# Kernel tuning notes

Hardware: AMD Instinct MI355X
Metric: run time of the kernel (lower is better)

## Reference

```python
import jax, jax.numpy as jnp
import numpy as np

LN_EPS = 1e-5  # torch LayerNorm default
K_NN = 5       # top-5 nearest patterns (simple-surprise path)


def setup_inputs() -> dict:
    key = jax.random.key(0)
    ks = jax.random.split(key, 5)
    B, S, D, M = 8, 8192, 256, 50
    return {
        "hidden_states": jax.random.normal(ks[0], (B, S, D), dtype=jnp.float32),
        "memory": jax.random.normal(ks[1], (M, D), dtype=jnp.float32),
        "W1": jax.random.normal(ks[2], (D, 2 * D), dtype=jnp.float32) * (1.0 / np.sqrt(D)),
        "b1": jnp.zeros((2 * D,), dtype=jnp.float32),
        "W2": jax.random.normal(ks[3], (2 * D, D), dtype=jnp.float32) * (1.0 / np.sqrt(2 * D)),
        "b2": jnp.zeros((D,), dtype=jnp.float32),
        "ln_gamma": jnp.ones((D,), dtype=jnp.float32),
        "ln_beta": jnp.zeros((D,), dtype=jnp.float32),
    }


def reference(hidden_states, memory, W1, b1, W2, b2, ln_gamma, ln_beta):
    # Feature extractor: Linear -> ReLU -> (Dropout, eval=identity) -> Linear -> LayerNorm
    h = jax.nn.relu(jnp.einsum("bsd,de->bse", hidden_states, W1) + b1)
    f = jnp.einsum("bse,ed->bsd", h, W2) + b2
    mu = jnp.mean(f, axis=-1, keepdims=True)
    var = jnp.var(f, axis=-1, keepdims=True)
    feats = (f - mu) * jax.lax.rsqrt(var + LN_EPS) * ln_gamma + ln_beta  # [B,S,D]

    # Simple-surprise path, vectorized over all (b, s) tokens:
    # L2 distance of each token feature to every memory pattern.
    f_sq = jnp.sum(feats * feats, axis=-1)      # [B,S]
    m_sq = jnp.sum(memory * memory, axis=-1)    # [M]
    dots = jnp.einsum("bsd,md->bsm", feats, memory)  # [B,S,M]
    d2 = jnp.maximum(f_sq[..., None] + m_sq - 2.0 * dots, 0.0)
    dists = jnp.sqrt(d2)                        # [B,S,M]

    # k smallest distances -> mean -> sigmoid(avg - 1)
    neg_knn, _ = jax.lax.top_k(-dists, K_NN)    # [B,S,K]
    avg_dist = -jnp.mean(neg_knn, axis=-1)      # [B,S]
    surprise_scores = jax.nn.sigmoid(avg_dist - 1.0)
    return surprise_scores
```

## Files before the change

kernel.cpp:

```cpp
#include <hip/hip_runtime.h>
#include <math.h>

typedef __attribute__((ext_vector_type(8))) short bf16x8;
typedef __attribute__((ext_vector_type(4))) float f32x4;

static __device__ __forceinline__ unsigned short f2b(float x) {
  unsigned int u = __float_as_uint(x);
  u += 0x7FFFu + ((u >> 16) & 1u);
  return (unsigned short)(u >> 16);
}

__global__ void prep_weights(const float* __restrict__ W1,
                             const float* __restrict__ W2,
                             const float* __restrict__ mem,
                             unsigned short* __restrict__ W1T,
                             unsigned short* __restrict__ W2T,
                             unsigned short* __restrict__ memB,
                             float* __restrict__ msq) {
  int i = blockIdx.x * 256 + threadIdx.x;
  if (i < 131072) {
    int k = i >> 9, n = i & 511;
    W1T[n * 256 + k] = f2b(W1[i]);
  } else if (i < 262144) {
    int j = i - 131072;
    int k = j >> 8, n = j & 255;
    W2T[n * 512 + k] = f2b(W2[j]);
  } else if (i < 278528) {
    int j = i - 262144;
    int r = j >> 8;
    memB[j] = (r < 50) ? f2b(mem[j]) : (unsigned short)0;
  } else {
    int t = threadIdx.x;
    int r = t >> 2, c0 = (t & 3) * 64;
    float s = 0.f;
    if (r < 50) {
      for (int c = 0; c < 64; ++c) {
        float v = mem[r * 256 + c0 + c];
        s += v * v;
      }
    }
    s += __shfl_xor(s, 1, 64);
    s += __shfl_xor(s, 2, 64);
    if ((t & 3) == 0) msq[r] = (r < 50) ? s : 1e30f;
  }
}

#define XP 264
#define HP 136
#define DPitch 53

__global__ __launch_bounds__(256, 3) void fused_main(
    const float* __restrict__ X, const float* __restrict__ b1v,
    const float* __restrict__ b2v, const float* __restrict__ gammav,
    const float* __restrict__ betav, const unsigned short* __restrict__ W1T,
    const unsigned short* __restrict__ W2T,
    const unsigned short* __restrict__ memB, const float* __restrict__ msq,
    float* __restrict__ out) {
  __shared__ __align__(16) char smem[51200];
  unsigned short* Xs = (unsigned short*)smem;
  unsigned short* Hs = (unsigned short*)(smem + 33792);
  float* distS = (float*)(smem + 33792);
  float* red = (float*)(smem + 47360);
  float* psum   = red;
  float* psumsq = red + 256;
  float* fsqp   = red + 512;
  float* muS    = red + 768;
  float* rstdS  = red + 832;
  float* fsqS   = red + 896;

  const int tid = threadIdx.x;
  const int wid = tid >> 6;
  const int lane = tid & 63;
  const int l16 = lane & 15;
  const int quad = lane >> 4;

  const float4* X4 = (const float4*)(X + (size_t)blockIdx.x * 64 * 256);
#pragma unroll
  for (int j = 0; j < 16; ++j) {
    int idx = j * 256 + tid;
    float4 v = X4[idx];
    int row = idx >> 6, c4 = (idx & 63) << 2;
    unsigned int p0 = f2b(v.x) | ((unsigned int)f2b(v.y) << 16);
    unsigned int p1 = f2b(v.z) | ((unsigned int)f2b(v.w) << 16);
    *(uint2*)(&Xs[row * XP + c4]) = make_uint2(p0, p1);
  }

  f32x4 acc2[4][4];
#pragma unroll
  for (int mt = 0; mt < 4; ++mt) {
    const float4 bb = *(const float4*)(&b2v[wid * 64 + mt * 16 + quad * 4]);
#pragma unroll
    for (int nt = 0; nt < 4; ++nt) {
      acc2[mt][nt][0] = bb.x; acc2[mt][nt][1] = bb.y;
      acc2[mt][nt][2] = bb.z; acc2[mt][nt][3] = bb.w;
    }
  }

  __syncthreads();

  for (int cc = 0; cc < 4; ++cc) {
    int hbase = cc * 128 + wid * 32;
    f32x4 acc1[2][4];
#pragma unroll
    for (int mt = 0; mt < 2; ++mt) {
      const float4 bb = *(const float4*)(&b1v[hbase + mt * 16 + quad * 4]);
#pragma unroll
      for (int nt = 0; nt < 4; ++nt) {
        acc1[mt][nt][0] = bb.x; acc1[mt][nt][1] = bb.y;
        acc1[mt][nt][2] = bb.z; acc1[mt][nt][3] = bb.w;
      }
    }
    bf16x8 a2p[2][4];
#pragma unroll
    for (int k2 = 0; k2 < 2; ++k2)
#pragma unroll
      for (int mt = 0; mt < 4; ++mt)
        a2p[k2][mt] = *(const bf16x8*)(W2T + (wid * 64 + mt * 16 + l16) * 512 +
                                       cc * 128 + k2 * 32 + quad * 8);
#pragma unroll
    for (int kk = 0; kk < 8; ++kk) {
      int k0 = kk * 32 + quad * 8;
      bf16x8 a[2], b[4];
#pragma unroll
      for (int mt = 0; mt < 2; ++mt)
        a[mt] = *(const bf16x8*)(W1T + (hbase + mt * 16 + l16) * 256 + k0);
#pragma unroll
      for (int nt = 0; nt < 4; ++nt)
        b[nt] = *(const bf16x8*)(Xs + (nt * 16 + l16) * XP + k0);
#pragma unroll
      for (int mt = 0; mt < 2; ++mt)
#pragma unroll
        for (int nt = 0; nt < 4; ++nt)
          acc1[mt][nt] = __builtin_amdgcn_mfma_f32_16x16x32_bf16(
              a[mt], b[nt], acc1[mt][nt], 0, 0, 0);
    }
    __syncthreads();
#pragma unroll
    for (int mt = 0; mt < 2; ++mt) {
#pragma unroll
      for (int nt = 0; nt < 4; ++nt) {
        int token = nt * 16 + l16;
        int hloc = wid * 32 + mt * 16 + quad * 4;
        f32x4 v = acc1[mt][nt];
        unsigned int p0 = f2b(fmaxf(v[0], 0.f)) | ((unsigned int)f2b(fmaxf(v[1], 0.f)) << 16);
        unsigned int p1 = f2b(fmaxf(v[2], 0.f)) | ((unsigned int)f2b(fmaxf(v[3], 0.f)) << 16);
        *(uint2*)(&Hs[token * HP + hloc]) = make_uint2(p0, p1);
      }
    }
    __syncthreads();
#pragma unroll
    for (int k2 = 0; k2 < 4; ++k2) {
      int k0 = k2 * 32 + quad * 8;
      bf16x8 a[4], b[4];
#pragma unroll
      for (int mt = 0; mt < 4; ++mt) {
        if (k2 < 2)
          a[mt] = a2p[k2][mt];
        else
          a[mt] = *(const bf16x8*)(W2T + (wid * 64 + mt * 16 + l16) * 512 +
                                   cc * 128 + k0 - quad * 8 + quad * 8);
      }
#pragma unroll
      for (int nt = 0; nt < 4; ++nt)
        b[nt] = *(const bf16x8*)(Hs + (nt * 16 + l16) * HP + k0);
#pragma unroll
      for (int mt = 0; mt < 4; ++mt)
#pragma unroll
        for (int nt = 0; nt < 4; ++nt)
          acc2[mt][nt] = __builtin_amdgcn_mfma_f32_16x16x32_bf16(
              a[mt], b[nt], acc2[mt][nt], 0, 0, 0);
    }
  }

  __syncthreads();

#pragma unroll
  for (int nt = 0; nt < 4; ++nt) {
    float s = 0.f, sq = 0.f;
#pragma unroll
    for (int mt = 0; mt < 4; ++mt)
#pragma unroll
      for (int r = 0; r < 4; ++r) {
        float v = acc2[mt][nt][r];
        s += v; sq += v * v;
      }
    s += __shfl_xor(s, 16, 64); sq += __shfl_xor(sq, 16, 64);
    s += __shfl_xor(s, 32, 64); sq += __shfl_xor(sq, 32, 64);
    if (quad == 0) {
      psum[wid * 64 + nt * 16 + l16] = s;
      psumsq[wid * 64 + nt * 16 + l16] = sq;
    }
  }
  __syncthreads();
  if (tid < 64) {
    float s = psum[tid] + psum[64 + tid] + psum[128 + tid] + psum[192 + tid];
    float sq = psumsq[tid] + psumsq[64 + tid] + psumsq[128 + tid] + psumsq[192 + tid];
    float mu = s * (1.f / 256.f);
    float var = sq * (1.f / 256.f) - mu * mu;
    muS[tid] = mu;
    rstdS[tid] = rsqrtf(var + 1e-5f);
  }
  __syncthreads();

  {
    float4 g[4], be[4];
#pragma unroll
    for (int mt = 0; mt < 4; ++mt) {
      g[mt]  = *(const float4*)(&gammav[wid * 64 + mt * 16 + quad * 4]);
      be[mt] = *(const float4*)(&betav[wid * 64 + mt * 16 + quad * 4]);
    }
#pragma unroll
    for (int nt = 0; nt < 4; ++nt) {
      int token = nt * 16 + l16;
      float mu = muS[token], rs = rstdS[token];
      float fs = 0.f;
#pragma unroll
      for (int mt = 0; mt < 4; ++mt) {
        float y0 = (acc2[mt][nt][0] - mu) * rs * g[mt].x + be[mt].x;
        float y1 = (acc2[mt][nt][1] - mu) * rs * g[mt].y + be[mt].y;
        float y2 = (acc2[mt][nt][2] - mu) * rs * g[mt].z + be[mt].z;
        float y3 = (acc2[mt][nt][3] - mu) * rs * g[mt].w + be[mt].w;
        fs += y0 * y0 + y1 * y1 + y2 * y2 + y3 * y3;
        unsigned int p0 = f2b(y0) | ((unsigned int)f2b(y1) << 16);
        unsigned int p1 = f2b(y2) | ((unsigned int)f2b(y3) << 16);
        *(uint2*)(&Xs[token * XP + wid * 64 + mt * 16 + quad * 4]) =
            make_uint2(p0, p1);
      }
      fs += __shfl_xor(fs, 16, 64);
      fs += __shfl_xor(fs, 32, 64);
      if (quad == 0) fsqp[wid * 64 + token] = fs;
    }
  }
  __syncthreads();
  if (tid < 64)
    fsqS[tid] = fsqp[tid] + fsqp[64 + tid] + fsqp[128 + tid] + fsqp[192 + tid];
  __syncthreads();

  f32x4 acc3[4];
#pragma unroll
  for (int nt = 0; nt < 4; ++nt) {
    acc3[nt][0] = 0.f; acc3[nt][1] = 0.f; acc3[nt][2] = 0.f; acc3[nt][3] = 0.f;
  }
#pragma unroll
  for (int kk = 0; kk < 8; ++kk) {
    int k0 = kk * 32 + quad * 8;
    bf16x8 a = *(const bf16x8*)(Xs + (wid * 16 + l16) * XP + k0);
#pragma unroll
    for (int nt = 0; nt < 4; ++nt) {
      bf16x8 b = *(const bf16x8*)(memB + (nt * 16 + l16) * 256 + k0);
      acc3[nt] = __builtin_amdgcn_mfma_f32_16x16x32_bf16(a, b, acc3[nt], 0, 0, 0);
    }
  }
  {
    float4 fsq4 = *(const float4*)(&fsqS[wid * 16 + quad * 4]);
#pragma unroll
    for (int nt = 0; nt < 4; ++nt) {
      int col = nt * 16 + l16;
      float mq = msq[col];
#pragma unroll
      for (int r = 0; r < 4; ++r) {
        float fv = (r == 0) ? fsq4.x : (r == 1) ? fsq4.y : (r == 2) ? fsq4.z : fsq4.w;
        float d2 = fv + mq - 2.f * acc3[nt][r];
        float d = sqrtf(fmaxf(d2, 0.f));
        int row = wid * 16 + quad * 4 + r;
        if (col < 50) distS[row * DPitch + col] = d;
      }
    }
  }
  __syncthreads();

  if (tid < 64) {
    float b0 = 1e30f, b1 = 1e30f, b2 = 1e30f, b3 = 1e30f, b4 = 1e30f;
    const float* dr = &distS[tid * DPitch];
    for (int j = 0; j < 50; ++j) {
      float v = dr[j];
      b4 = fminf(b4, v);
      float t;
      if (b4 < b3) { t = b3; b3 = b4; b4 = t; }
      if (b3 < b2) { t = b2; b2 = b3; b3 = t; }
      if (b2 < b1) { t = b1; b1 = b2; b2 = t; }
      if (b1 < b0) { t = b0; b0 = b1; b1 = t; }
    }
    float avg = (b0 + b1 + b2 + b3 + b4) * 0.2f;
    float sarg = avg - 1.f;
    out[blockIdx.x * 64 + tid] = 1.f / (1.f + __expf(-sarg));
  }
}

extern "C" void kernel_launch(void* const* d_in, const int* in_sizes, int n_in,
                              void* d_out, int out_size, void* d_ws, size_t ws_size,
                              hipStream_t stream) {
  const float* X   = (const float*)d_in[0];
  const float* mem = (const float*)d_in[1];
  const float* W1  = (const float*)d_in[2];
  const float* b1  = (const float*)d_in[3];
  const float* W2  = (const float*)d_in[4];
  const float* b2  = (const float*)d_in[5];
  const float* g   = (const float*)d_in[6];
  const float* be  = (const float*)d_in[7];
  float* out = (float*)d_out;

  unsigned short* W1T  = (unsigned short*)d_ws;
  unsigned short* W2T  = W1T + 131072;
  unsigned short* memB = W2T + 131072;
  float* msq = (float*)(memB + 16384);

  prep_weights<<<1089, 256, 0, stream>>>(W1, W2, mem, W1T, W2T, memB, msq);
  fused_main<<<1024, 256, 0, stream>>>(X, b1, b2, g, be, W1T, W2T, memB, msq, out);
}
```

Before: 215.4 us.

## Swizzle LDS tiles, shrink shared memory and hidden chunk to raise occupancy

Replaces the padded X and H shared-memory tiles with unpadded XOR-swizzled layouts. This cuts LDS per block from 51200 to 40960 bytes, and launch bounds are raised to 4 blocks per SIMD. The hidden dimension is now processed in 8 chunks of 64 instead of 4 chunks of 128, and the W2 prefetch registers are dropped. Together these lower register and LDS pressure for higher occupancy. In exchange there are more barrier-separated chunk iterations, and a sync is added because distS now aliases the X tile.

```diff
diff --git a/kernel.cpp b/kernel.cpp
--- a/kernel.cpp
+++ b/kernel.cpp
@@ -45,22 +45,20 @@
   }
 }
 
-#define XP 264
-#define HP 136
 #define DPitch 53
 
-__global__ __launch_bounds__(256, 3) void fused_main(
+#define SWZ(b, r) ((b) ^ (((r) & 7) << 4))
+
+__global__ __launch_bounds__(256, 4) void fused_main(
     const float* __restrict__ X, const float* __restrict__ b1v,
     const float* __restrict__ b2v, const float* __restrict__ gammav,
     const float* __restrict__ betav, const unsigned short* __restrict__ W1T,
     const unsigned short* __restrict__ W2T,
     const unsigned short* __restrict__ memB, const float* __restrict__ msq,
     float* __restrict__ out) {
-  __shared__ __align__(16) char smem[51200];
-  unsigned short* Xs = (unsigned short*)smem;
-  unsigned short* Hs = (unsigned short*)(smem + 33792);
-  float* distS = (float*)(smem + 33792);
-  float* red = (float*)(smem + 47360);
+  __shared__ __align__(16) char smem[40960];
+  float* distS = (float*)smem;
+  float* red = (float*)(smem + 32768);
   float* psum   = red;
   float* psumsq = red + 256;
   float* fsqp   = red + 512;
@@ -68,6 +66,9 @@
   float* rstdS  = red + 832;
   float* fsqS   = red + 896;
 
+  const char* W1Tc = (const char*)W1T;
+  const char* W2Tc = (const char*)W2T;
+
   const int tid = threadIdx.x;
   const int wid = tid >> 6;
   const int lane = tid & 63;
@@ -77,12 +78,11 @@
   const float4* X4 = (const float4*)(X + (size_t)blockIdx.x * 64 * 256);
 #pragma unroll
   for (int j = 0; j < 16; ++j) {
-    int idx = j * 256 + tid;
-    float4 v = X4[idx];
-    int row = idx >> 6, c4 = (idx & 63) << 2;
+    int row = j * 4 + wid;
+    float4 v = X4[row * 64 + lane];
     unsigned int p0 = f2b(v.x) | ((unsigned int)f2b(v.y) << 16);
     unsigned int p1 = f2b(v.z) | ((unsigned int)f2b(v.w) << 16);
-    *(uint2*)(&Xs[row * XP + c4]) = make_uint2(p0, p1);
+    *(uint2*)(smem + SWZ(row * 512 + lane * 8, row)) = make_uint2(p0, p1);
   }
 
   f32x4 acc2[4][4];
@@ -98,71 +98,54 @@
 
   __syncthreads();
 
-  for (int cc = 0; cc < 4; ++cc) {
-    int hbase = cc * 128 + wid * 32;
-    f32x4 acc1[2][4];
-#pragma unroll
-    for (int mt = 0; mt < 2; ++mt) {
-      const float4 bb = *(const float4*)(&b1v[hbase + mt * 16 + quad * 4]);
+  for (int cc = 0; cc < 8; ++cc) {
+    int hbase = cc * 64 + wid * 16;
+    f32x4 acc1[4];
+    {
+      const float4 bb = *(const float4*)(&b1v[hbase + quad * 4]);
 #pragma unroll
       for (int nt = 0; nt < 4; ++nt) {
-        acc1[mt][nt][0] = bb.x; acc1[mt][nt][1] = bb.y;
-        acc1[mt][nt][2] = bb.z; acc1[mt][nt][3] = bb.w;
-      }
-    }
-    bf16x8 a2p[2][4];
-#pragma unroll
-    for (int k2 = 0; k2 < 2; ++k2)
+        acc1[nt][0] = bb.x; acc1[nt][1] = bb.y;
+        acc1[nt][2] = bb.z; acc1[nt][3] = bb.w;
+      }
+    }
+#pragma unroll
+    for (int kk = 0; kk < 8; ++kk) {
+      int kb = kk * 64 + quad * 16;
+      bf16x8 a = *(const bf16x8*)(W1Tc + (hbase + l16) * 512 + kb);
+      bf16x8 b[4];
+#pragma unroll
+      for (int nt = 0; nt < 4; ++nt) {
+        int r = nt * 16 + l16;
+        b[nt] = *(const bf16x8*)(smem + SWZ(r * 512 + kb, r));
+      }
+#pragma unroll
+      for (int nt = 0; nt < 4; ++nt)
+        acc1[nt] = __builtin_amdgcn_mfma_f32_16x16x32_bf16(a, b[nt], acc1[nt], 0, 0, 0);
+    }
+    __syncthreads();
+#pragma unroll
+    for (int nt = 0; nt < 4; ++nt) {
+      int token = nt * 16 + l16;
+      f32x4 v = acc1[nt];
+      unsigned int p0 = f2b(fmaxf(v[0], 0.f)) | ((unsigned int)f2b(fmaxf(v[1], 0.f)) << 16);
+      unsigned int p1 = f2b(fmaxf(v[2], 0.f)) | ((unsigned int)f2b(fmaxf(v[3], 0.f)) << 16);
+      *(uint2*)(smem + 32768 + SWZ(token * 128 + wid * 32 + quad * 8, token)) =
+          make_uint2(p0, p1);
+    }
+    __syncthreads();
+#pragma unroll
+    for (int k2 = 0; k2 < 2; ++k2) {
+      bf16x8 a[4], b[4];
 #pragma unroll
       for (int mt = 0; mt < 4; ++mt)
-        a2p[k2][mt] = *(const bf16x8*)(W2T + (wid * 64 + mt * 16 + l16) * 512 +
-                                       cc * 128 + k2 * 32 + quad * 8);
-#pragma unroll
-    for (int kk = 0; kk < 8; ++kk) {
-      int k0 = kk * 32 + quad * 8;
-      bf16x8 a[2], b[4];
-#pragma unroll
-      for (int mt = 0; mt < 2; ++mt)
-        a[mt] = *(const bf16x8*)(W1T + (hbase + mt * 16 + l16) * 256 + k0);
-#pragma unroll
-      for (int nt = 0; nt < 4; ++nt)
-        b[nt] = *(const bf16x8*)(Xs + (nt * 16 + l16) * XP + k0);
-#pragma unroll
-      for (int mt = 0; mt < 2; ++mt)
-#pragma unroll
-        for (int nt = 0; nt < 4; ++nt)
-          acc1[mt][nt] = __builtin_amdgcn_mfma_f32_16x16x32_bf16(
-              a[mt], b[nt], acc1[mt][nt], 0, 0, 0);
-    }
-    __syncthreads();
-#pragma unroll
-    for (int mt = 0; mt < 2; ++mt) {
+        a[mt] = *(const bf16x8*)(W2Tc + (wid * 64 + mt * 16 + l16) * 1024 +
+                                 cc * 128 + k2 * 64 + quad * 16);
 #pragma unroll
       for (int nt = 0; nt < 4; ++nt) {
-        int token = nt * 16 + l16;
-        int hloc = wid * 32 + mt * 16 + quad * 4;
-        f32x4 v = acc1[mt][nt];
-        unsigned int p0 = f2b(fmaxf(v[0], 0.f)) | ((unsigned int)f2b(fmaxf(v[1], 0.f)) << 16);
-        unsigned int p1 = f2b(fmaxf(v[2], 0.f)) | ((unsigned int)f2b(fmaxf(v[3], 0.f)) << 16);
-        *(uint2*)(&Hs[token * HP + hloc]) = make_uint2(p0, p1);
-      }
-    }
-    __syncthreads();
-#pragma unroll
-    for (int k2 = 0; k2 < 4; ++k2) {
-      int k0 = k2 * 32 + quad * 8;
-      bf16x8 a[4], b[4];
-#pragma unroll
-      for (int mt = 0; mt < 4; ++mt) {
-        if (k2 < 2)
-          a[mt] = a2p[k2][mt];
-        else
-          a[mt] = *(const bf16x8*)(W2T + (wid * 64 + mt * 16 + l16) * 512 +
-                                   cc * 128 + k0 - quad * 8 + quad * 8);
-      }
-#pragma unroll
-      for (int nt = 0; nt < 4; ++nt)
-        b[nt] = *(const bf16x8*)(Hs + (nt * 16 + l16) * HP + k0);
+        int r = nt * 16 + l16;
+        b[nt] = *(const bf16x8*)(smem + 32768 + SWZ(r * 128 + k2 * 64 + quad * 16, r));
+      }
 #pragma unroll
       for (int mt = 0; mt < 4; ++mt)
 #pragma unroll
@@ -223,7 +206,7 @@
         fs += y0 * y0 + y1 * y1 + y2 * y2 + y3 * y3;
         unsigned int p0 = f2b(y0) | ((unsigned int)f2b(y1) << 16);
         unsigned int p1 = f2b(y2) | ((unsigned int)f2b(y3) << 16);
-        *(uint2*)(&Xs[token * XP + wid * 64 + mt * 16 + quad * 4]) =
+        *(uint2*)(smem + SWZ(token * 512 + wid * 128 + mt * 32 + quad * 8, token)) =
             make_uint2(p0, p1);
       }
       fs += __shfl_xor(fs, 16, 64);
@@ -243,14 +226,17 @@
   }
 #pragma unroll
   for (int kk = 0; kk < 8; ++kk) {
+    int kb = kk * 64 + quad * 16;
+    int ar = wid * 16 + l16;
+    bf16x8 a = *(const bf16x8*)(smem + SWZ(ar * 512 + kb, ar));
     int k0 = kk * 32 + quad * 8;
-    bf16x8 a = *(const bf16x8*)(Xs + (wid * 16 + l16) * XP + k0);
 #pragma unroll
     for (int nt = 0; nt < 4; ++nt) {
       bf16x8 b = *(const bf16x8*)(memB + (nt * 16 + l16) * 256 + k0);
       acc3[nt] = __builtin_amdgcn_mfma_f32_16x16x32_bf16(a, b, acc3[nt], 0, 0, 0);
     }
   }
+  __syncthreads();
   {
     float4 fsq4 = *(const float4*)(&fsqS[wid * 16 + quad * 4]);
 #pragma unroll
```

After: 215.6 us. Within noise of the previous version (+0.1%).
